# Performance work log

Hardware: AMD Instinct MI355X
Metric: run time of the kernel (lower is better)

The kernel has to match this reference:

```python
import jax, jax.numpy as jnp
import numpy as np

NEMB = 512
NEMBDIM = 64
NHIDDEN = 1024
NINPUT = 784
COMMIT_COST = 0.25


def setup_inputs() -> dict:
    key = jax.random.key(0)
    ks = jax.random.split(key, 16)
    B = 32768
    x = jax.random.uniform(ks[0], (B, NINPUT), dtype=jnp.float32)
    # codebook: uniform(-1/nemb, 1/nemb) as in torch init
    emb = jax.random.uniform(ks[1], (NEMB, NEMBDIM), dtype=jnp.float32,
                             minval=-1.0 / NEMB, maxval=1.0 / NEMB)
    s = 0.02
    We1 = jax.random.normal(ks[2], (NHIDDEN, NINPUT), dtype=jnp.float32) * s
    be1 = jnp.zeros((NHIDDEN,), jnp.float32)
    We2 = jax.random.normal(ks[3], (NHIDDEN, NHIDDEN), dtype=jnp.float32) * s
    be2 = jnp.zeros((NHIDDEN,), jnp.float32)
    We3 = jax.random.normal(ks[4], (NEMBDIM, NHIDDEN), dtype=jnp.float32) * s
    be3 = jnp.zeros((NEMBDIM,), jnp.float32)
    Wd1 = jax.random.normal(ks[5], (NHIDDEN, NEMBDIM), dtype=jnp.float32) * s
    bd1 = jnp.zeros((NHIDDEN,), jnp.float32)
    Wd2 = jax.random.normal(ks[6], (NHIDDEN, NHIDDEN), dtype=jnp.float32) * s
    bd2 = jnp.zeros((NHIDDEN,), jnp.float32)
    Wd3 = jax.random.normal(ks[7], (NINPUT, NHIDDEN), dtype=jnp.float32) * s
    bd3 = jnp.zeros((NINPUT,), jnp.float32)
    return dict(x=x, emb=emb, We1=We1, be1=be1, We2=We2, be2=be2, We3=We3, be3=be3,
                Wd1=Wd1, bd1=bd1, Wd2=Wd2, bd2=bd2, Wd3=Wd3, bd3=bd3)


def reference(x, emb, We1, be1, We2, be2, We3, be3, Wd1, bd1, Wd2, bd2, Wd3, bd3):
    # Encoder MLP (dropout inactive at inference)
    h = jax.nn.relu(x @ We1.T + be1)
    h = jax.nn.relu(h @ We2.T + be2)
    z = h @ We3.T + be3  # [B, nembdim]

    # VQ codebook lookup. NOTE: original code omits the factor 2 on the cross
    # term (sum(z^2) + sum(e^2) - z @ e.T); we reproduce it faithfully.
    d = (jnp.sum(z * z, axis=1, keepdims=True)
         + jnp.sum(emb * emb, axis=1)
         - z @ emb.T)  # [B, nemb]
    idx = jnp.argmin(d, axis=1)  # [B]
    q = emb[idx]  # gather == one-hot @ emb, same math

    code_loss = jnp.mean((q - jax.lax.stop_gradient(z)) ** 2)
    commit_loss = jnp.mean((jax.lax.stop_gradient(q) - z) ** 2)
    loss = code_loss + COMMIT_COST * commit_loss

    # straight-through estimator
    q_st = z + jax.lax.stop_gradient(q - z)

    # Decoder MLP
    h = jax.nn.relu(q_st @ Wd1.T + bd1)
    h = jax.nn.relu(h @ Wd2.T + bd2)
    out = jax.nn.sigmoid(h @ Wd3.T + bd3)
    return out, loss
```

## Files before the change

kernel.cpp:

```cpp
#include <hip/hip_runtime.h>
#include <stdint.h>
#include <stddef.h>

typedef __bf16 bf16x8 __attribute__((ext_vector_type(8)));
typedef float  f32x4  __attribute__((ext_vector_type(4)));
typedef unsigned short u16;
typedef unsigned char  u8;

#define NIN   784
#define NINP  896
#define NH    1024
#define NE    512
#define ND    64
#define NOUTP 1024

#define BAR()   asm volatile("s_barrier" ::: "memory")
#define LGKM0() asm volatile("s_waitcnt lgkmcnt(0)" ::: "memory")
#define VM4()   asm volatile("s_waitcnt vmcnt(4)" ::: "memory")
#define VM3()   asm volatile("s_waitcnt vmcnt(3)" ::: "memory")
#define VM0()   asm volatile("s_waitcnt vmcnt(0)" ::: "memory")
#define FSWZ(r) (((r) ^ ((r) >> 2)) & 3)
#define GLDS(g, l) __builtin_amdgcn_global_load_lds((__attribute__((address_space(1))) void*)(g), (__attribute__((address_space(3))) void*)(l), 16, 0, 0)

static __device__ __forceinline__ u16 f2bf(float f) {
  union { float f; unsigned u; } v; v.f = f;
  unsigned r = v.u + 0x7fffu + ((v.u >> 16) & 1u);
  return (u16)(r >> 16);
}
static __device__ __forceinline__ float bf2f(u16 b) {
  union { unsigned u; float f; } v; v.u = ((unsigned)b) << 16; return v.f;
}
static __device__ __forceinline__ unsigned pack4fp8(float a, float b, float c, float d) {
  unsigned p;
  asm("v_cvt_pk_fp8_f32 %0, %1, %2" : "=v"(p) : "v"(a), "v"(b));
  asm("v_cvt_pk_fp8_f32 %0, %1, %2 op_sel:[0,0,1]" : "+v"(p) : "v"(c), "v"(d));
  return p;
}
static __device__ __forceinline__ u8 f2fp8(float a) {
  unsigned p;
  asm("v_cvt_pk_fp8_f32 %0, %1, %2" : "=v"(p) : "v"(a), "v"(a));
  return (u8)(p & 0xff);
}


__global__ void cast_tiled8(const float* __restrict__ src, u8* __restrict__ dst,
                            int R, int C, int Cp) {
  int r = blockIdx.y;
  int c4 = (blockIdx.x * blockDim.x + threadIdx.x) * 4;
  if (c4 >= Cp) return;
  unsigned o = 0;
  if (r < R && c4 < C) {
    const float4 v = *(const float4*)&src[(size_t)r * C + c4];
    o = pack4fp8(v.x, v.y, v.z, v.w);
  }
  size_t off = ((size_t)(r >> 8) * (Cp >> 6) + (c4 >> 6)) * 16384
             + ((r & 255) << 6) + ((((c4 >> 4) & 3) ^ FSWZ(r)) << 4) + (c4 & 15);
  *(unsigned*)&dst[off] = o;
}

__global__ void cast_rm8(const float* __restrict__ src, u8* __restrict__ dst, int R, int C) {
  int r = blockIdx.y;
  int c4 = (blockIdx.x * blockDim.x + threadIdx.x) * 4;
  if (c4 >= C) return;
  const float4 v = *(const float4*)&src[(size_t)r * C + c4];
  *(unsigned*)&dst[(size_t)r * C + c4] = pack4fp8(v.x, v.y, v.z, v.w);
}

__global__ void emb_prep(const float* __restrict__ emb, u16* __restrict__ ebf,
                         float* __restrict__ cvec) {
  int j = blockIdx.x, l = threadIdx.x;
  float v = emb[j * ND + l];
  ebf[j * 64 + (((l >> 3) ^ (j & 7)) << 3) + (l & 7)] = f2bf(v);
  float s = v * v;
  #pragma unroll
  for (int off = 32; off > 0; off >>= 1) s += __shfl_down(s, off);
  if (l == 0) cvec[j] = s;
}

template <int ACT, int OMODE, bool NCHK>
__global__ __launch_bounds__(256, 3)
void gemm128f8(const u8* __restrict__ A, const u8* __restrict__ Bm,
               const float* __restrict__ bias, float* __restrict__ Cf,
               u8* __restrict__ Cb, int N, int K, int ldc, int ntiles) {
  __shared__ __attribute__((aligned(128))) u8 lds[32768];
  const int tid = threadIdx.x, lane = tid & 63, w = tid >> 6;
  const int wr = w >> 1, wc = w & 1;
  const int lr = lane & 15, hi = lane >> 4;

  int nwg = gridDim.x, cpx = nwg >> 3, b = blockIdx.x;
  int sb = (b & 7) * cpx + (b >> 3);
  int tm = sb / ntiles, tn = sb % ntiles;

  const int NT = K >> 6;
  const u8* Ap = A + (size_t)(tm >> 1) * NT * 16384 + (size_t)(tm & 1) * 8192;
  const u8* Bp = Bm + (size_t)(tn >> 1) * NT * 16384 + (size_t)(tn & 1) * 8192;

  auto stage = [&](int t, int buf) {
    #pragma unroll
    for (int i = 0; i < 2; ++i)
      GLDS(Ap + (size_t)t * 16384 + ((i * 256 + tid) << 4),
           lds + buf * 8192 + ((i * 256 + w * 64) << 4));
    #pragma unroll
    for (int i = 0; i < 2; ++i)
      GLDS(Bp + (size_t)t * 16384 + ((i * 256 + tid) << 4),
           lds + 16384 + buf * 8192 + ((i * 256 + w * 64) << 4));
  };

  f32x4 acc[4][4] = {};
  stage(0, 0);
  if (NT > 1) stage(1, 1);

  for (int t = 0; t < NT; ++t) {
    const int buf = t & 1;
    if (t + 1 < NT) { VM4(); } else { VM0(); }
    BAR();
    const u8* lA = lds + buf * 8192;
    const u8* lB = lds + 16384 + buf * 8192;
    long af[4][2], bfr[4][2];
    #pragma unroll
    for (int m = 0; m < 4; ++m) {
      int row = wr * 64 + m * 16 + lr;
      #pragma unroll
      for (int e = 0; e < 2; ++e) {
        int ch = (e * 2 + (hi >> 1)) ^ FSWZ(row);
        af[m][e] = *(const long*)&lA[row * 64 + ch * 16 + ((hi & 1) << 3)];
      }
    }
    #pragma unroll
    for (int n = 0; n < 4; ++n) {
      int row = wc * 64 + n * 16 + lr;
      #pragma unroll
      for (int e = 0; e < 2; ++e) {
        int ch = (e * 2 + (hi >> 1)) ^ FSWZ(row);
        bfr[n][e] = *(const long*)&lB[row * 64 + ch * 16 + ((hi & 1) << 3)];
      }
    }
    LGKM0();
    BAR();
    if (t + 2 < NT) stage(t + 2, buf);
    #pragma unroll
    for (int m = 0; m < 4; ++m)
      #pragma unroll
      for (int n = 0; n < 4; ++n)
        #pragma unroll
        for (int e = 0; e < 2; ++e)
          acc[m][n] = __builtin_amdgcn_mfma_f32_16x16x32_fp8_fp8(
              af[m][e], bfr[n][e], acc[m][n], 0, 0, 0);
  }

  const int c0 = wc * 64;
  float bv[4];
  #pragma unroll
  for (int n = 0; n < 4; ++n) {
    int col = tn * 128 + c0 + n * 16 + lr;
    bv[n] = (!NCHK || col < N) ? bias[col] : 0.f;
  }
  float* lf = (float*)lds;
  #pragma unroll
  for (int p = 0; p < 2; ++p) {
    __syncthreads();
    if (wr == p) {
      #pragma unroll
      for (int m = 0; m < 4; ++m)
        #pragma unroll
        for (int j = 0; j < 4; ++j) {
          int lrow = m * 16 + hi * 4 + j;
          #pragma unroll
          for (int n = 0; n < 4; ++n) {
            int col = c0 + n * 16 + lr;
            float v = acc[m][n][j] + bv[n];
            if (ACT == 1) v = fmaxf(v, 0.f);
            if (ACT == 2) v = 1.f / (1.f + __expf(-v));
            lf[lrow * 128 + (((col >> 2) ^ (lrow & 31)) << 2) + (col & 3)] = v;
          }
        }
    }
    __syncthreads();
    #pragma unroll
    for (int it = 0; it < 2; ++it) {
      int idx = it * 256 + tid;
      int lrow = idx >> 3, cc = idx & 7;
      f32x4 q[4];
      #pragma unroll
      for (int s = 0; s < 4; ++s)
        q[s] = *(const f32x4*)&lf[lrow * 128 + (((cc * 4 + s) ^ (lrow & 31)) << 2)];
      int R = tm * 128 + p * 64 + lrow;
      if (OMODE == 1) {
        int C = tn * 128 + cc * 16;
        int4 o;
        o.x = pack4fp8(q[0][0], q[0][1], q[0][2], q[0][3]);
        o.y = pack4fp8(q[1][0], q[1][1], q[1][2], q[1][3]);
        o.z = pack4fp8(q[2][0], q[2][1], q[2][2], q[2][3]);
        o.w = pack4fp8(q[3][0], q[3][1], q[3][2], q[3][3]);
        size_t off = ((size_t)(R >> 8) * (ldc >> 6) + (C >> 6)) * 16384
                   + ((R & 255) << 6) + ((((C >> 4) & 3) ^ FSWZ(R)) << 4);
        *(int4*)&Cb[off] = o;
      } else {
        int gc = tn * 128 + cc * 16;
        if (!NCHK || gc < N) {
          #pragma unroll
          for (int s = 0; s < 4; ++s)
            *(f32x4*)&Cf[(size_t)R * ldc + gc + s * 4] = q[s];
        }
      }
    }
  }
}

__global__ __launch_bounds__(256, 1)
void z_vq(const u8* __restrict__ Atiled,
          const u8* __restrict__ Wrm,
          const float* __restrict__ be3,
          const u16* __restrict__ ebf,
          const float* __restrict__ cvec,
          u8* __restrict__ qb8, float* __restrict__ lossacc) {
  __shared__ u8 lsA[2][128 * 64];
  __shared__ u8 lsW[2][64 * 64];
  __shared__ u16 embl[512 * 64];
  __shared__ float zls[128 * 68];
  __shared__ int bidxl[128];

  const int t = threadIdx.x;
  const int lane = t & 63;
  const int w = t >> 6;
  const int lr = lane & 15, hi = lane >> 4;
  const int tm = blockIdx.x;

  #pragma unroll
  for (int i = 0; i < 16; ++i) {
    const u16* g = ebf + (size_t)((i * 256 + t) << 3);
    u16* l = embl + (size_t)((i * 256 + w * 64) << 3);
    GLDS(g, l);
  }

  const size_t abase0 = ((size_t)(tm >> 1) * 16) * 16384 + (size_t)(tm & 1) * 8192;
  auto stageA = [&](int kt, int buf) {
    #pragma unroll
    for (int i = 0; i < 2; ++i) {
      const u8* g = Atiled + abase0 + (size_t)kt * 16384 + ((i * 256 + t) << 4);
      u8* l = lsA[buf] + ((i * 256 + w * 64) << 4);
      GLDS(g, l);
    }
  };
  auto stageW = [&](int kt, int buf) {
    int row = w * 16 + (lane >> 2), p = lane & 3;
    const u8* g = Wrm + (size_t)row * 1024 + kt * 64 + ((p ^ FSWZ(row)) << 4);
    u8* l = lsW[buf] + ((w * 64) << 4);
    GLDS(g, l);
  };

  f32x4 acc[2][4] = {};
  stageA(0, 0); stageW(0, 0);
  stageA(1, 1); stageW(1, 1);
  for (int kt = 0; kt < 16; ++kt) {
    const int bf = kt & 1;
    if (kt < 15) { VM3(); } else { VM0(); }
    BAR();
    #pragma unroll
    for (int kk = 0; kk < 64; kk += 32) {
      long af[2], bfr[4];
      #pragma unroll
      for (int m = 0; m < 2; ++m) {
        int row = w * 32 + m * 16 + lr;
        int ch = ((kk >> 4) + (hi >> 1)) ^ FSWZ(row);
        af[m] = *(const long*)&lsA[bf][row * 64 + ch * 16 + ((hi & 1) << 3)];
      }
      #pragma unroll
      for (int n = 0; n < 4; ++n) {
        int row = n * 16 + lr;
        int ch = ((kk >> 4) + (hi >> 1)) ^ FSWZ(row);
        bfr[n] = *(const long*)&lsW[bf][row * 64 + ch * 16 + ((hi & 1) << 3)];
      }
      #pragma unroll
      for (int m = 0; m < 2; ++m)
        #pragma unroll
        for (int n = 0; n < 4; ++n)
          acc[m][n] = __builtin_amdgcn_mfma_f32_16x16x32_fp8_fp8(af[m], bfr[n], acc[m][n], 0, 0, 0);
    }
    LGKM0();
    BAR();
    if (kt + 2 < 16) { stageA(kt + 2, bf); stageW(kt + 2, bf); }
  }

  #pragma unroll
  for (int m = 0; m < 2; ++m)
    #pragma unroll
    for (int j = 0; j < 4; ++j) {
      int row = w * 32 + m * 16 + hi * 4 + j;
      #pragma unroll
      for (int n = 0; n < 4; ++n) {
        int col = n * 16 + lr;
        zls[row * 68 + col] = acc[m][n][j] + be3[col];
      }
    }
  __syncthreads();

  bf16x8 azf[2][2];
  #pragma unroll
  for (int rt = 0; rt < 2; ++rt)
    #pragma unroll
    for (int kf = 0; kf < 2; ++kf) {
      int row = w * 32 + rt * 16 + lr;
      union { bf16x8 v; u16 u[8]; } pk;
      #pragma unroll
      for (int e = 0; e < 8; ++e)
        pk.u[e] = f2bf(zls[row * 68 + kf * 32 + hi * 8 + e]);
      azf[rt][kf] = pk.v;
    }

  float bvv[2][4]; int bii[2][4];
  #pragma unroll
  for (int rt = 0; rt < 2; ++rt)
    #pragma unroll
    for (int j = 0; j < 4; ++j) { bvv[rt][j] = 3.4e38f; bii[rt][j] = 0; }

  for (int ct = 0; ct < 32; ++ct) {
    bf16x8 bqf[2];
    #pragma unroll
    for (int kf = 0; kf < 2; ++kf) {
      int row = ct * 16 + lr;
      int ch = (kf * 4 + hi) ^ (row & 7);
      bqf[kf] = *(const bf16x8*)&embl[row * 64 + ch * 8];
    }
    float cv = cvec[ct * 16 + lr];
    #pragma unroll
    for (int rt = 0; rt < 2; ++rt) {
      f32x4 sc = {};
      sc = __builtin_amdgcn_mfma_f32_16x16x32_bf16(azf[rt][0], bqf[0], sc, 0, 0, 0);
      sc = __builtin_amdgcn_mfma_f32_16x16x32_bf16(azf[rt][1], bqf[1], sc, 0, 0, 0);
      int code = ct * 16 + lr;
      #pragma unroll
      for (int j = 0; j < 4; ++j) {
        float d = cv - sc[j];
        if (d < bvv[rt][j]) { bvv[rt][j] = d; bii[rt][j] = code; }
      }
    }
  }
  #pragma unroll
  for (int off = 1; off < 16; off <<= 1) {
    #pragma unroll
    for (int rt = 0; rt < 2; ++rt)
      #pragma unroll
      for (int j = 0; j < 4; ++j) {
        float ov = __shfl_xor(bvv[rt][j], off);
        int   oi = __shfl_xor(bii[rt][j], off);
        if (ov < bvv[rt][j] || (ov == bvv[rt][j] && oi < bii[rt][j])) {
          bvv[rt][j] = ov; bii[rt][j] = oi;
        }
      }
  }
  if (lr == 0) {
    #pragma unroll
    for (int rt = 0; rt < 2; ++rt)
      #pragma unroll
      for (int j = 0; j < 4; ++j)
        bidxl[w * 32 + rt * 16 + hi * 4 + j] = bii[rt][j];
  }
  __syncthreads();

  const int gr0 = tm * 128;
  float ls = 0.f;
  #pragma unroll 4
  for (int r8 = 0; r8 < 32; ++r8) {
    int row = w * 32 + r8;
    int bi = bidxl[row];
    u16 qu = embl[bi * 64 + (((lane >> 3) ^ (bi & 7)) << 3) + (lane & 7)];
    float qf = bf2f(qu);
    float d = qf - zls[row * 68 + lane];
    ls += d * d;
    int R = gr0 + row;
    qb8[(size_t)R * 64 + ((((lane >> 4) & 3) ^ FSWZ(R)) << 4) + (lane & 15)] = f2fp8(qf);
  }
  #pragma unroll
  for (int off = 32; off > 0; off >>= 1) ls += __shfl_down(ls, off);
  if (lane == 0) atomicAdd(lossacc, ls);
}

__global__ void loss_final(const float* __restrict__ acc, float* __restrict__ o, float denom) {
  o[0] = acc[0] * 1.25f / denom;
}

extern "C" void kernel_launch(void* const* d_in, const int* in_sizes, int n_in,
                              void* d_out, int out_size, void* d_ws, size_t ws_size,
                              hipStream_t stream) {
  const float* x   = (const float*)d_in[0];
  const float* emb = (const float*)d_in[1];
  const float* We1 = (const float*)d_in[2];
  const float* be1 = (const float*)d_in[3];
  const float* We2 = (const float*)d_in[4];
  const float* be2 = (const float*)d_in[5];
  const float* We3 = (const float*)d_in[6];
  const float* be3 = (const float*)d_in[7];
  const float* Wd1 = (const float*)d_in[8];
  const float* bd1 = (const float*)d_in[9];
  const float* Wd2 = (const float*)d_in[10];
  const float* bd2 = (const float*)d_in[11];
  const float* Wd3 = (const float*)d_in[12];
  const float* bd3 = (const float*)d_in[13];

  const int Bn = in_sizes[0] / NIN;
  float* out = (float*)d_out;
  float* out_loss = out + (size_t)Bn * NIN;

  char* ws = (char*)d_ws;
  size_t off = 0;
  auto take = [&](size_t bytes) { char* p = ws + off; off += (bytes + 255) & ~(size_t)255; return p; };

  u8*    xpad8 = (u8*)take((size_t)Bn * NINP);
  u8*    hA8   = (u8*)take((size_t)Bn * NH);
  u8*    hB8   = (u8*)take((size_t)Bn * NH);
  u8*    qb8   = (u8*)take((size_t)Bn * ND);
  u8*    we1p8 = (u8*)take((size_t)NH * NINP);
  u8*    we2b8 = (u8*)take((size_t)NH * NH);
  u8*    we3r8 = (u8*)take((size_t)64 * NH);
  u8*    wd1b8 = (u8*)take((size_t)NH * ND);
  u8*    wd2b8 = (u8*)take((size_t)NH * NH);
  u8*    wd3p8 = (u8*)take((size_t)NOUTP * NH);
  u16*   embb  = (u16*)take((size_t)NE * ND * 2);
  float* cvec  = (float*)take(NE * 4);
  float* lossa = (float*)take(4);

  hipMemsetAsync(lossa, 0, 4, stream);

  cast_tiled8<<<dim3(1, Bn),    256, 0, stream>>>(x,   xpad8, Bn,  NIN, NINP);
  cast_tiled8<<<dim3(1, NH),    256, 0, stream>>>(We1, we1p8, NH,  NIN, NINP);
  cast_tiled8<<<dim3(1, NH),    256, 0, stream>>>(We2, we2b8, NH,  NH,  NH);
  cast_rm8   <<<dim3(1, 64),    256, 0, stream>>>(We3, we3r8, 64,  NH);
  cast_tiled8<<<dim3(1, NH),    256, 0, stream>>>(Wd1, wd1b8, NH,  ND,  ND);
  cast_tiled8<<<dim3(1, NH),    256, 0, stream>>>(Wd2, wd2b8, NH,  NH,  NH);
  cast_tiled8<<<dim3(1, NOUTP), 256, 0, stream>>>(Wd3, wd3p8, NIN, NH,  NH);
  emb_prep<<<NE, 64, 0, stream>>>(emb, embb, cvec);

  const int mt = Bn / 128;
  gemm128f8<1,1,false><<<mt * 8, 256, 0, stream>>>(xpad8, we1p8, be1, nullptr, hA8, NH, NINP, NH, 8);
  gemm128f8<1,1,false><<<mt * 8, 256, 0, stream>>>(hA8, we2b8, be2, nullptr, hB8, NH, NH, NH, 8);
  z_vq<<<Bn / 128, 256, 0, stream>>>(hB8, we3r8, be3, embb, cvec, qb8, lossa);
  gemm128f8<1,1,false><<<mt * 8, 256, 0, stream>>>(qb8, wd1b8, bd1, nullptr, hA8, NH, 64, NH, 8);
  gemm128f8<1,1,false><<<mt * 8, 256, 0, stream>>>(hA8, wd2b8, bd2, nullptr, hB8, NH, NH, NH, 8);
  gemm128f8<2,0,true ><<<mt * 7, 256, 0, stream>>>(hB8, wd3p8, bd3, out, nullptr, NIN, NH, NIN, 7);

  loss_final<<<1, 1, 0, stream>>>(lossa, out_loss, (float)Bn * ND);
}
```

Before: 310.0 us.

## Switch FP8 GEMMs to scaled 32x32x64 MFMA with direct fp32 epilogue

```diff
diff --git a/kernel.cpp b/kernel.cpp
--- a/kernel.cpp
+++ b/kernel.cpp
@@ -4,6 +4,8 @@
 
 typedef __bf16 bf16x8 __attribute__((ext_vector_type(8)));
 typedef float  f32x4  __attribute__((ext_vector_type(4)));
+typedef float  f32x16 __attribute__((ext_vector_type(16)));
+typedef int    i32x8  __attribute__((ext_vector_type(8)));
 typedef unsigned short u16;
 typedef unsigned char  u8;
 
@@ -20,6 +22,7 @@
 #define VM3()   asm volatile("s_waitcnt vmcnt(3)" ::: "memory")
 #define VM0()   asm volatile("s_waitcnt vmcnt(0)" ::: "memory")
 #define FSWZ(r) (((r) ^ ((r) >> 2)) & 3)
+#define SCL1    0x7F7F7F7F
 #define GLDS(g, l) __builtin_amdgcn_global_load_lds((__attribute__((address_space(1))) void*)(g), (__attribute__((address_space(3))) void*)(l), 16, 0, 0)
 
 static __device__ __forceinline__ u16 f2bf(float f) {
@@ -79,13 +82,13 @@
 
 template <int ACT, int OMODE, bool NCHK>
 __global__ __launch_bounds__(256, 3)
-void gemm128f8(const u8* __restrict__ A, const u8* __restrict__ Bm,
+void gemm128mx(const u8* __restrict__ A, const u8* __restrict__ Bm,
                const float* __restrict__ bias, float* __restrict__ Cf,
                u8* __restrict__ Cb, int N, int K, int ldc, int ntiles) {
   __shared__ __attribute__((aligned(128))) u8 lds[32768];
   const int tid = threadIdx.x, lane = tid & 63, w = tid >> 6;
   const int wr = w >> 1, wc = w & 1;
-  const int lr = lane & 15, hi = lane >> 4;
+  const int l31 = lane & 31, h = lane >> 5;
 
   int nwg = gridDim.x, cpx = nwg >> 3, b = blockIdx.x;
   int sb = (b & 7) * cpx + (b >> 3);
@@ -106,7 +109,7 @@
            lds + 16384 + buf * 8192 + ((i * 256 + w * 64) << 4));
   };
 
-  f32x4 acc[4][4] = {};
+  f32x16 acc[2][2] = {};
   stage(0, 0);
   if (NT > 1) stage(1, 1);
 
@@ -116,76 +119,91 @@
     BAR();
     const u8* lA = lds + buf * 8192;
     const u8* lB = lds + 16384 + buf * 8192;
-    long af[4][2], bfr[4][2];
-    #pragma unroll
-    for (int m = 0; m < 4; ++m) {
-      int row = wr * 64 + m * 16 + lr;
-      #pragma unroll
-      for (int e = 0; e < 2; ++e) {
-        int ch = (e * 2 + (hi >> 1)) ^ FSWZ(row);
-        af[m][e] = *(const long*)&lA[row * 64 + ch * 16 + ((hi & 1) << 3)];
-      }
-    }
-    #pragma unroll
-    for (int n = 0; n < 4; ++n) {
-      int row = wc * 64 + n * 16 + lr;
-      #pragma unroll
-      for (int e = 0; e < 2; ++e) {
-        int ch = (e * 2 + (hi >> 1)) ^ FSWZ(row);
-        bfr[n][e] = *(const long*)&lB[row * 64 + ch * 16 + ((hi & 1) << 3)];
-      }
+    i32x8 af[2], bf_[2];
+    #pragma unroll
+    for (int s = 0; s < 2; ++s) {
+      int row = wr * 64 + s * 32 + l31;
+      int F = FSWZ(row);
+      const u8* base = lA + row * 64;
+      int4 lo = *(const int4*)&base[(((h << 1)    ) ^ F) << 4];
+      int4 hi = *(const int4*)&base[(((h << 1) | 1) ^ F) << 4];
+      af[s][0] = lo.x; af[s][1] = lo.y; af[s][2] = lo.z; af[s][3] = lo.w;
+      af[s][4] = hi.x; af[s][5] = hi.y; af[s][6] = hi.z; af[s][7] = hi.w;
+    }
+    #pragma unroll
+    for (int s = 0; s < 2; ++s) {
+      int row = wc * 64 + s * 32 + l31;
+      int F = FSWZ(row);
+      const u8* base = lB + row * 64;
+      int4 lo = *(const int4*)&base[(((h << 1)    ) ^ F) << 4];
+      int4 hi = *(const int4*)&base[(((h << 1) | 1) ^ F) << 4];
+      bf_[s][0] = lo.x; bf_[s][1] = lo.y; bf_[s][2] = lo.z; bf_[s][3] = lo.w;
+      bf_[s][4] = hi.x; bf_[s][5] = hi.y; bf_[s][6] = hi.z; bf_[s][7] = hi.w;
     }
     LGKM0();
     BAR();
     if (t + 2 < NT) stage(t + 2, buf);
     #pragma unroll
-    for (int m = 0; m < 4; ++m)
-      #pragma unroll
-      for (int n = 0; n < 4; ++n)
+    for (int ms = 0; ms < 2; ++ms)
+      #pragma unroll
+      for (int ns = 0; ns < 2; ++ns)
+        acc[ms][ns] = __builtin_amdgcn_mfma_scale_f32_32x32x64_f8f6f4(
+            af[ms], bf_[ns], acc[ms][ns], 0, 0, 0, SCL1, 0, SCL1);
+  }
+
+  float bv[2];
+  #pragma unroll
+  for (int ns = 0; ns < 2; ++ns) {
+    int col = tn * 128 + wc * 64 + ns * 32 + l31;
+    bv[ns] = (!NCHK || col < N) ? bias[col] : 0.f;
+  }
+
+  if (OMODE == 0) {
+    #pragma unroll
+    for (int ms = 0; ms < 2; ++ms)
+      #pragma unroll
+      for (int r = 0; r < 16; ++r) {
+        int row = tm * 128 + wr * 64 + ms * 32 + (r & 3) + ((r >> 2) << 3) + (h << 2);
         #pragma unroll
-        for (int e = 0; e < 2; ++e)
-          acc[m][n] = __builtin_amdgcn_mfma_f32_16x16x32_fp8_fp8(
-              af[m][e], bfr[n][e], acc[m][n], 0, 0, 0);
-  }
-
-  const int c0 = wc * 64;
-  float bv[4];
-  #pragma unroll
-  for (int n = 0; n < 4; ++n) {
-    int col = tn * 128 + c0 + n * 16 + lr;
-    bv[n] = (!NCHK || col < N) ? bias[col] : 0.f;
-  }
-  float* lf = (float*)lds;
-  #pragma unroll
-  for (int p = 0; p < 2; ++p) {
-    __syncthreads();
-    if (wr == p) {
-      #pragma unroll
-      for (int m = 0; m < 4; ++m)
+        for (int ns = 0; ns < 2; ++ns) {
+          int col = tn * 128 + wc * 64 + ns * 32 + l31;
+          if (NCHK && col >= N) continue;
+          float v = acc[ms][ns][r] + bv[ns];
+          if (ACT == 1) v = fmaxf(v, 0.f);
+          if (ACT == 2) v = 1.f / (1.f + __expf(-v));
+          Cf[(size_t)row * ldc + col] = v;
+        }
+      }
+  } else {
+    float* lf = (float*)lds;
+    #pragma unroll
+    for (int p = 0; p < 2; ++p) {
+      __syncthreads();
+      if (wr == p) {
         #pragma unroll
-        for (int j = 0; j < 4; ++j) {
-          int lrow = m * 16 + hi * 4 + j;
+        for (int ms = 0; ms < 2; ++ms)
           #pragma unroll
-          for (int n = 0; n < 4; ++n) {
-            int col = c0 + n * 16 + lr;
-            float v = acc[m][n][j] + bv[n];
-            if (ACT == 1) v = fmaxf(v, 0.f);
-            if (ACT == 2) v = 1.f / (1.f + __expf(-v));
-            lf[lrow * 128 + (((col >> 2) ^ (lrow & 31)) << 2) + (col & 3)] = v;
+          for (int r = 0; r < 16; ++r) {
+            int lrow = ms * 32 + (r & 3) + ((r >> 2) << 3) + (h << 2);
+            #pragma unroll
+            for (int ns = 0; ns < 2; ++ns) {
+              int col = wc * 64 + ns * 32 + l31;
+              float v = acc[ms][ns][r] + bv[ns];
+              if (ACT == 1) v = fmaxf(v, 0.f);
+              lf[lrow * 128 + (((col >> 2) ^ (lrow & 31)) << 2) + (col & 3)] = v;
+            }
           }
-        }
-    }
-    __syncthreads();
-    #pragma unroll
-    for (int it = 0; it < 2; ++it) {
-      int idx = it * 256 + tid;
-      int lrow = idx >> 3, cc = idx & 7;
-      f32x4 q[4];
-      #pragma unroll
-      for (int s = 0; s < 4; ++s)
-        q[s] = *(const f32x4*)&lf[lrow * 128 + (((cc * 4 + s) ^ (lrow & 31)) << 2)];
-      int R = tm * 128 + p * 64 + lrow;
-      if (OMODE == 1) {
+      }
+      __syncthreads();
+      #pragma unroll
+      for (int it = 0; it < 2; ++it) {
+        int idx = it * 256 + tid;
+        int lrow = idx >> 3, cc = idx & 7;
+        f32x4 q[4];
+        #pragma unroll
+        for (int s = 0; s < 4; ++s)
+          q[s] = *(const f32x4*)&lf[lrow * 128 + (((cc * 4 + s) ^ (lrow & 31)) << 2)];
+        int R = tm * 128 + p * 64 + lrow;
         int C = tn * 128 + cc * 16;
         int4 o;
         o.x = pack4fp8(q[0][0], q[0][1], q[0][2], q[0][3]);
@@ -195,13 +213,6 @@
         size_t off = ((size_t)(R >> 8) * (ldc >> 6) + (C >> 6)) * 16384
                    + ((R & 255) << 6) + ((((C >> 4) & 3) ^ FSWZ(R)) << 4);
         *(int4*)&Cb[off] = o;
-      } else {
-        int gc = tn * 128 + cc * 16;
-        if (!NCHK || gc < N) {
-          #pragma unroll
-          for (int s = 0; s < 4; ++s)
-            *(f32x4*)&Cf[(size_t)R * ldc + gc + s * 4] = q[s];
-        }
       }
     }
   }
@@ -432,12 +443,12 @@
   emb_prep<<<NE, 64, 0, stream>>>(emb, embb, cvec);
 
   const int mt = Bn / 128;
-  gemm128f8<1,1,false><<<mt * 8, 256, 0, stream>>>(xpad8, we1p8, be1, nullptr, hA8, NH, NINP, NH, 8);
-  gemm128f8<1,1,false><<<mt * 8, 256, 0, stream>>>(hA8, we2b8, be2, nullptr, hB8, NH, NH, NH, 8);
+  gemm128mx<1,1,false><<<mt * 8, 256, 0, stream>>>(xpad8, we1p8, be1, nullptr, hA8, NH, NINP, NH, 8);
+  gemm128mx<1,1,false><<<mt * 8, 256, 0, stream>>>(hA8, we2b8, be2, nullptr, hB8, NH, NH, NH, 8);
   z_vq<<<Bn / 128, 256, 0, stream>>>(hB8, we3r8, be3, embb, cvec, qb8, lossa);
-  gemm128f8<1,1,false><<<mt * 8, 256, 0, stream>>>(qb8, wd1b8, bd1, nullptr, hA8, NH, 64, NH, 8);
-  gemm128f8<1,1,false><<<mt * 8, 256, 0, stream>>>(hA8, wd2b8, bd2, nullptr, hB8, NH, NH, NH, 8);
-  gemm128f8<2,0,true ><<<mt * 7, 256, 0, stream>>>(hB8, wd3p8, bd3, out, nullptr, NIN, NH, NIN, 7);
+  gemm128mx<1,1,false><<<mt * 8, 256, 0, stream>>>(qb8, wd1b8, bd1, nullptr, hA8, NH, 64, NH, 8);
+  gemm128mx<1,1,false><<<mt * 8, 256, 0, stream>>>(hA8, wd2b8, bd2, nullptr, hB8, NH, NH, NH, 8);
+  gemm128mx<2,0,true ><<<mt * 7, 256, 0, stream>>>(hB8, wd3p8, bd3, out, nullptr, NIN, NH, NIN, 7);
 
   loss_final<<<1, 1, 0, stream>>>(lossa, out_loss, (float)Bn * ND);
 }
```

After: 264.6 us. 14.7% less time.
